# Performance work log

Measured on AMD Instinct MI355X. Metric: run time of the kernel, lower is better.

Reference implementation:

```python
import jax, jax.numpy as jnp
import numpy as np

EMBED_DIM = 1024
NUM_HEADS = 16
HEAD_DIM = EMBED_DIM // NUM_HEADS


def setup_inputs() -> dict:
    key = jax.random.key(0)
    ks = jax.random.split(key, 9)
    B, T, D = 2, 4096, EMBED_DIM
    scale = 1.0 / np.sqrt(D)
    x = jax.random.normal(ks[0], (B, T, D), dtype=jnp.float32)
    # nn.Linear weights stored as (out, in); we use (in, out) layout via transpose-free init
    Wq = jax.random.uniform(ks[1], (D, D), dtype=jnp.float32, minval=-scale, maxval=scale)
    Wk = jax.random.uniform(ks[2], (D, D), dtype=jnp.float32, minval=-scale, maxval=scale)
    Wv = jax.random.uniform(ks[3], (D, D), dtype=jnp.float32, minval=-scale, maxval=scale)
    Wo = jax.random.uniform(ks[4], (D, D), dtype=jnp.float32, minval=-scale, maxval=scale)
    bq = jax.random.uniform(ks[5], (D,), dtype=jnp.float32, minval=-scale, maxval=scale)
    bk = jax.random.uniform(ks[6], (D,), dtype=jnp.float32, minval=-scale, maxval=scale)
    bv = jax.random.uniform(ks[7], (D,), dtype=jnp.float32, minval=-scale, maxval=scale)
    bo = jax.random.uniform(ks[8], (D,), dtype=jnp.float32, minval=-scale, maxval=scale)
    return {"x": x, "Wq": Wq, "bq": bq, "Wk": Wk, "bk": bk,
            "Wv": Wv, "bv": bv, "Wo": Wo, "bo": bo}


def reference(x, Wq, bq, Wk, bk, Wv, bv, Wo, bo):
    B, T, D = x.shape
    H, Hd = NUM_HEADS, HEAD_DIM
    q = x @ Wq + bq  # [B,T,D]
    k = x @ Wk + bk
    v = x @ Wv + bv
    # [B,T,D] -> [B,H,T,Hd]
    q = q.reshape(B, T, H, Hd).transpose(0, 2, 1, 3)
    k = k.reshape(B, T, H, Hd).transpose(0, 2, 1, 3)
    v = v.reshape(B, T, H, Hd).transpose(0, 2, 1, 3)
    att = jnp.einsum('bhqd,bhkd->bhqk', q, k) / jnp.sqrt(jnp.float32(Hd))
    causal = jnp.tril(jnp.ones((T, T), dtype=bool))  # True = keep
    att = jnp.where(causal, att, -jnp.inf)
    att = jax.nn.softmax(att, axis=-1)
    out = jnp.einsum('bhqk,bhkd->bhqd', att, v)  # [B,H,T,Hd]
    out = out.transpose(0, 2, 1, 3).reshape(B, T, D)
    return out @ Wo + bo
```

## Files before the change

kernel.cpp:

```cpp
#include <hip/hip_runtime.h>
#include <hip/hip_bf16.h>
#include <math.h>

typedef __bf16 bf16;
typedef __attribute__((ext_vector_type(8))) __bf16 bf16x8;
typedef __attribute__((ext_vector_type(4))) __bf16 bf16x4;
typedef __attribute__((ext_vector_type(4))) short short4v;
typedef __attribute__((ext_vector_type(4))) float f32x4;

#define MFMA16(a,b,c)  __builtin_amdgcn_mfma_f32_16x16x32_bf16((a),(b),(c),0,0,0)
#define MFMAK16(a,b,c) __builtin_amdgcn_mfma_f32_16x16x16bf16_1k((a),(b),(c),0,0,0)

__device__ __forceinline__ void gload16(const void* gp, void* lp) {
  __builtin_amdgcn_global_load_lds(
      (const __attribute__((address_space(1))) void*)gp,
      (__attribute__((address_space(3))) void*)lp, 16, 0, 0);
}

__global__ __launch_bounds__(256) void cast_x(
    const float* __restrict__ x, bf16* __restrict__ xb)
{
  size_t i = ((size_t)blockIdx.x*256 + threadIdx.x) * 8;
  f32x4 a = *(const f32x4*)(x+i);
  f32x4 b = *(const f32x4*)(x+i+4);
  bf16x8 o;
  #pragma unroll
  for (int j=0;j<4;j++) { o[j] = (bf16)a[j]; o[4+j] = (bf16)b[j]; }
  *(bf16x8*)(xb+i) = o;
}

__global__ __launch_bounds__(1024) void tr_cast(
    const float* __restrict__ w0, const float* __restrict__ w1,
    const float* __restrict__ w2, bf16* __restrict__ dst)
{
  __shared__ bf16 tile[64][65];
  const float* src = (blockIdx.z==0)?w0:(blockIdx.z==1)?w1:w2;
  bf16* d = dst + (size_t)blockIdx.z * (1024*1024);
  int x = threadIdx.x, y = threadIdx.y;
  int tc = blockIdx.x, tr = blockIdx.y;
  #pragma unroll
  for (int i=0;i<4;i++) {
    int r = y + i*16;
    tile[r][x] = (bf16)src[(size_t)(tr*64+r)*1024 + tc*64 + x];
  }
  __syncthreads();
  #pragma unroll
  for (int i=0;i<4;i++) {
    int r = y + i*16;
    d[(size_t)(tc*64+r)*1024 + tr*64 + x] = tile[x][r];
  }
}

__global__ __launch_bounds__(1024) void v_tr(
    const bf16* __restrict__ v, bf16* __restrict__ vt)
{
  __shared__ bf16 tile[64][65];
  int x = threadIdx.x, y = threadIdx.y;
  int tt = blockIdx.x;
  int bh = blockIdx.y;
  int b = bh >> 4, h = bh & 15;
  const bf16* src = v + ((size_t)b*4096 + tt*64)*1024 + h*64;
  bf16* dst = vt + ((size_t)bh*64)*4096 + tt*64;
  #pragma unroll
  for (int i=0;i<4;i++) {
    int r = y + i*16;
    tile[r][x] = src[(size_t)r*1024 + x];
  }
  __syncthreads();
  #pragma unroll
  for (int i=0;i<4;i++) {
    int r = y + i*16;
    dst[(size_t)r*4096 + x] = tile[x][r];
  }
}

__global__ __launch_bounds__(256) void gemm_qkv(
    const bf16* __restrict__ A, const bf16* __restrict__ Bt,
    const float* __restrict__ bq, const float* __restrict__ bk, const float* __restrict__ bv,
    bf16* __restrict__ q, bf16* __restrict__ k, bf16* __restrict__ v,
    int M, int K)
{
  __shared__ __align__(16) bf16 As[128*64];
  __shared__ __align__(16) bf16 Bs[128*64];
  const int tid  = threadIdx.x;
  const int wave = tid >> 6;
  const int lane = tid & 63;
  const int l15  = lane & 15;
  const int quad = lane >> 4;
  const int m0 = blockIdx.y * 128;
  const int n0 = blockIdx.x * 128;
  const int wm = (wave >> 1) * 64;
  const int wn = (wave & 1) * 64;

  int srow[4], scol[4];
  #pragma unroll
  for (int p=0;p<4;p++) {
    int cid = p*256 + tid;
    srow[p] = cid >> 3;
    scol[p] = ((cid & 7) ^ (srow[p] & 7)) << 3;
  }
  const int swz8 = l15 & 7;
  int rdo[2];
  #pragma unroll
  for (int kk=0;kk<2;kk++) rdo[kk] = (((kk*4 + quad) ^ swz8) << 3);

  f32x4 acc[4][4];
  #pragma unroll
  for (int i=0;i<4;i++)
    #pragma unroll
    for (int j=0;j<4;j++)
      acc[i][j] = (f32x4){0.f,0.f,0.f,0.f};

  for (int k0 = 0; k0 < K; k0 += 64) {
    __syncthreads();
    #pragma unroll
    for (int p=0;p<4;p++) {
      int cid = p*256 + tid;
      gload16(A  + (size_t)(m0+srow[p])*K + k0 + scol[p], As + cid*8);
      gload16(Bt + (size_t)(n0+srow[p])*K + k0 + scol[p], Bs + cid*8);
    }
    __syncthreads();
    #pragma unroll
    for (int kk=0;kk<2;kk++) {
      bf16x8 af[4], bfr[4];
      #pragma unroll
      for (int t=0;t<4;t++) {
        af[t]  = *(const bf16x8*)(As + (wm + t*16 + l15)*64 + rdo[kk]);
        bfr[t] = *(const bf16x8*)(Bs + (wn + t*16 + l15)*64 + rdo[kk]);
      }
      #pragma unroll
      for (int mt=0;mt<4;mt++)
        #pragma unroll
        for (int nt=0;nt<4;nt++)
          acc[mt][nt] = MFMA16(af[mt], bfr[nt], acc[mt][nt]);
    }
  }

  const int mat = n0 >> 10;
  const float* bsel = (mat==0) ? bq : (mat==1) ? bk : bv;
  bf16*       osel  = (mat==0) ? q  : (mat==1) ? k  : v;
  const float qsc   = (mat==0) ? 0.1803368801f : 1.0f;
  #pragma unroll
  for (int nt=0;nt<4;nt++) {
    int col = n0 + wn + nt*16 + l15;
    int cw  = col & 1023;
    float bvv = bsel[cw];
    #pragma unroll
    for (int mt=0;mt<4;mt++) {
      int row = m0 + wm + mt*16 + quad*4;
      #pragma unroll
      for (int r=0;r<4;r++)
        osel[(size_t)(row + r)*1024 + cw] = (bf16)((acc[mt][nt][r] + bvv) * qsc);
    }
  }
}

__global__ __launch_bounds__(256, 4) void gemm_out(
    const bf16* __restrict__ A, const bf16* __restrict__ Bt,
    const float* __restrict__ bias, float* __restrict__ C,
    int M, int N, int K)
{
  __shared__ __align__(16) bf16 As[128*64];
  __shared__ __align__(16) bf16 Bs[64*64];
  const int tid  = threadIdx.x;
  const int wave = tid >> 6;
  const int lane = tid & 63;
  const int l15  = lane & 15;
  const int quad = lane >> 4;
  const int m0 = blockIdx.y * 128;
  const int n0 = blockIdx.x * 64;
  const int wm = (wave >> 1) * 64;
  const int wn = (wave & 1) * 32;

  int srow[4], scol[4];
  #pragma unroll
  for (int p=0;p<4;p++) {
    int cid = p*256 + tid;
    srow[p] = cid >> 3;
    scol[p] = ((cid & 7) ^ (srow[p] & 7)) << 3;
  }
  const int swz8 = l15 & 7;
  int rdo[2];
  #pragma unroll
  for (int kk=0;kk<2;kk++) rdo[kk] = (((kk*4 + quad) ^ swz8) << 3);

  f32x4 acc[4][2];
  #pragma unroll
  for (int i=0;i<4;i++)
    #pragma unroll
    for (int j=0;j<2;j++)
      acc[i][j] = (f32x4){0.f,0.f,0.f,0.f};

  for (int k0 = 0; k0 < K; k0 += 64) {
    __syncthreads();
    #pragma unroll
    for (int p=0;p<4;p++)
      gload16(A + (size_t)(m0+srow[p])*K + k0 + scol[p], As + (p*256+tid)*8);
    #pragma unroll
    for (int p=0;p<2;p++) {
      int cid = p*256 + tid;
      gload16(Bt + (size_t)(n0+srow[p])*K + k0 + scol[p], Bs + cid*8);
    }
    __syncthreads();
    #pragma unroll
    for (int kk=0;kk<2;kk++) {
      bf16x8 af[4], bfr[2];
      #pragma unroll
      for (int t=0;t<4;t++)
        af[t]  = *(const bf16x8*)(As + (wm + t*16 + l15)*64 + rdo[kk]);
      #pragma unroll
      for (int t=0;t<2;t++)
        bfr[t] = *(const bf16x8*)(Bs + (wn + t*16 + l15)*64 + rdo[kk]);
      #pragma unroll
      for (int mt=0;mt<4;mt++)
        #pragma unroll
        for (int nt=0;nt<2;nt++)
          acc[mt][nt] = MFMA16(af[mt], bfr[nt], acc[mt][nt]);
    }
  }

  #pragma unroll
  for (int nt=0;nt<2;nt++) {
    int col = n0 + wn + nt*16 + l15;
    float bvv = bias[col];
    #pragma unroll
    for (int mt=0;mt<4;mt++) {
      int row = m0 + wm + mt*16 + quad*4;
      #pragma unroll
      for (int r=0;r<4;r++)
        C[(size_t)(row + r)*N + col] = acc[mt][nt][r] + bvv;
    }
  }
}

__global__ __launch_bounds__(256, 2) void attn_fwd(
    const bf16* __restrict__ Q, const bf16* __restrict__ Kp,
    const bf16* __restrict__ Vtg, bf16* __restrict__ O)
{
  __shared__ __align__(16) char KsB[4*8192];
  __shared__ __align__(16) char VtB[4*8192];

  const int tid  = threadIdx.x;
  const int w    = tid >> 6;
  const int lane = tid & 63;
  const int l15  = lane & 15;
  const int quad = lane >> 4;

  const int bid = blockIdx.x;
  const int pp  = bid >> 5;
  const int bh  = bid & 31;
  const int h   = bh & 15;
  const int b   = bh >> 4;

  const size_t headoff = (size_t)h * 64;
  const size_t bbase   = (size_t)b * 4096;

  short4v ones_s;
  {
    bf16x4 o1;
    #pragma unroll
    for (int j=0;j<4;j++) o1[j] = (bf16)1.0f;
    ones_s = __builtin_bit_cast(short4v, o1);
  }

  const int kt_row = tid >> 2;
  const int kswz   = (kt_row & 7) << 4;
  const int ks_w0  = kt_row*128 + (((tid & 3)*32)      ^ kswz);
  const int ks_w1  = kt_row*128 + (((tid & 3)*32 + 16) ^ kswz);

  const int vd  = tid >> 2;
  const int vt0 = (tid & 3) * 16;
  int vw[4];
  #pragma unroll
  for (int u=0;u<4;u++)
    vw[u] = vd*128 + (((vt0 + u*4)*2) ^ ((vd & 15) << 3));

  const int s7    = l15 & 7;
  const int ks_r0 = l15*128 + ((quad ^ (s7 & 3)) << 4) + ((s7 >> 2) << 6);
  const int ks_r1 = ks_r0 ^ 64;
  const int vt_rbase = l15*128 + ((quad ^ (l15 & 3)) << 3) + ((l15 >> 2) << 5);
  int vt_r[4];
  #pragma unroll
  for (int tt=0;tt<4;tt++) vt_r[tt] = vt_rbase ^ (tt << 5);

  const bf16* kbase0 = Kp  + (bbase + kt_row)*1024 + headoff + (tid & 3)*16;
  const bf16* vbase0 = Vtg + ((size_t)(bh*64) + vd)*4096 + vt0;

  for (int ph = 0; ph < 2; ++ph) {
    const int qt = ph ? (31 - pp) : pp;
    const int q0 = qt * 128;
    const int ktmax = 2*qt + 1;

    bf16x8 aqA[2], aqB[2];
    {
      int rowA = q0 + w*16 + l15;
      const bf16* qp = Q + (bbase + rowA)*1024 + headoff + quad*8;
      aqA[0] = *(const bf16x8*)(qp);
      aqA[1] = *(const bf16x8*)(qp + 32);
      qp += 64*1024;
      aqB[0] = *(const bf16x8*)(qp);
      aqB[1] = *(const bf16x8*)(qp + 32);
    }

    f32x4 accoA[4], accoB[4], accliA, accliB;
    #pragma unroll
    for (int i=0;i<4;i++) { accoA[i] = (f32x4){0.f,0.f,0.f,0.f}; accoB[i] = (f32x4){0.f,0.f,0.f,0.f}; }
    accliA = (f32x4){0.f,0.f,0.f,0.f};
    accliB = (f32x4){0.f,0.f,0.f,0.f};

    __syncthreads();
    #pragma unroll
    for (int j=0;j<2;j++) {
      const bf16* kp = kbase0 + (size_t)j*64*1024;
      const bf16* vp = vbase0 + j*64;
      bf16x8 k0 = *(const bf16x8*)(kp);
      bf16x8 k1 = *(const bf16x8*)(kp + 8);
      bf16x8 v0 = *(const bf16x8*)(vp);
      bf16x8 v1 = *(const bf16x8*)(vp + 8);
      char* ksn = KsB + j*8192;
      char* vtn = VtB + j*8192;
      *(bf16x8*)(ksn + ks_w0) = k0;
      *(bf16x8*)(ksn + ks_w1) = k1;
      *(bf16x4*)(vtn + vw[0]) = __builtin_shufflevector(v0, v0, 0,1,2,3);
      *(bf16x4*)(vtn + vw[1]) = __builtin_shufflevector(v0, v0, 4,5,6,7);
      *(bf16x4*)(vtn + vw[2]) = __builtin_shufflevector(v1, v1, 0,1,2,3);
      *(bf16x4*)(vtn + vw[3]) = __builtin_shufflevector(v1, v1, 4,5,6,7);
    }
    __syncthreads();

    const bf16* kpref = kbase0 + (size_t)2*64*1024;
    const bf16* vpref = vbase0 + 128;

    for (int kt = 0; kt <= ktmax; ++kt) {
      const bool pre = (kt + 2 <= ktmax);

      bf16x8 kr0, kr1, vr0, vr1;
      if (pre) {
        kr0 = *(const bf16x8*)(kpref);
        kr1 = *(const bf16x8*)(kpref + 8);
        vr0 = *(const bf16x8*)(vpref);
        vr1 = *(const bf16x8*)(vpref + 8);
        kpref += 64*1024;
        vpref += 64;
      }

      const char* ksb = KsB + (kt & 3)*8192;
      const char* vtb = VtB + (kt & 3)*8192;

      f32x4 accsA[4], accsB[4];
      #pragma unroll
      for (int i=0;i<4;i++) { accsA[i] = (f32x4){0.f,0.f,0.f,0.f}; accsB[i] = (f32x4){0.f,0.f,0.f,0.f}; }

      __builtin_amdgcn_s_setprio(1);
      #pragma unroll
      for (int kk=0;kk<2;kk++) {
        #pragma unroll
        for (int tt=0;tt<4;tt++) {
          bf16x8 ka = *(const bf16x8*)(ksb + (kk ? ks_r1 : ks_r0) + tt*2048);
          accsA[tt] = MFMA16(ka, aqA[kk], accsA[tt]);
          accsB[tt] = MFMA16(ka, aqB[kk], accsB[tt]);
        }
      }
      __builtin_amdgcn_s_setprio(0);

      short4v ptsA[4], ptsB[4];
      if (kt < 2*qt) {
        #pragma unroll
        for (int tt=0;tt<4;tt++) {
          bf16x4 pa, pb;
          #pragma unroll
          for (int r=0;r<4;r++) {
            pa[r] = (bf16)__builtin_amdgcn_exp2f(accsA[tt][r]);
            pb[r] = (bf16)__builtin_amdgcn_exp2f(accsB[tt][r]);
          }
          ptsA[tt] = __builtin_bit_cast(short4v, pa);
          ptsB[tt] = __builtin_bit_cast(short4v, pb);
        }
      } else {
        const bool adead = (kt > 2*qt);
        #pragma unroll
        for (int tt=0;tt<4;tt++) {
          bf16x4 pa, pb;
          #pragma unroll
          for (int r=0;r<4;r++) {
            const bool tq = (tt*16 + quad*4 + r > w*16 + l15);
            float fa = __builtin_amdgcn_exp2f(accsA[tt][r]);
            if (adead || tq) fa = 0.0f;
            float fb = __builtin_amdgcn_exp2f(accsB[tt][r]);
            if (adead && tq) fb = 0.0f;
            pa[r] = (bf16)fa; pb[r] = (bf16)fb;
          }
          ptsA[tt] = __builtin_bit_cast(short4v, pa);
          ptsB[tt] = __builtin_bit_cast(short4v, pb);
        }
      }

      __builtin_amdgcn_s_setprio(1);
      #pragma unroll
      for (int nt=0;nt<4;nt++) {
        #pragma unroll
        for (int tt=0;tt<4;tt++) {
          bf16x4 va = *(const bf16x4*)(vtb + vt_r[tt] + nt*2048);
          short4v vas = __builtin_bit_cast(short4v, va);
          accoA[nt] = MFMAK16(vas, ptsA[tt], accoA[nt]);
          accoB[nt] = MFMAK16(vas, ptsB[tt], accoB[nt]);
        }
      }
      #pragma unroll
      for (int tt=0;tt<4;tt++) {
        accliA = MFMAK16(ones_s, ptsA[tt], accliA);
        accliB = MFMAK16(ones_s, ptsB[tt], accliB);
      }
      __builtin_amdgcn_s_setprio(0);

      if (pre) {
        char* ksn = KsB + ((kt + 2) & 3)*8192;
        char* vtn = VtB + ((kt + 2) & 3)*8192;
        *(bf16x8*)(ksn + ks_w0) = kr0;
        *(bf16x8*)(ksn + ks_w1) = kr1;
        *(bf16x4*)(vtn + vw[0]) = __builtin_shufflevector(vr0, vr0, 0,1,2,3);
        *(bf16x4*)(vtn + vw[1]) = __builtin_shufflevector(vr0, vr0, 4,5,6,7);
        *(bf16x4*)(vtn + vw[2]) = __builtin_shufflevector(vr1, vr1, 0,1,2,3);
        *(bf16x4*)(vtn + vw[3]) = __builtin_shufflevector(vr1, vr1, 4,5,6,7);
      }
      if (kt & 1) __syncthreads();
    }

    {
      float invA = 1.0f / accliA[0];
      float invB = 1.0f / accliB[0];
      int rowA = q0 + w*16 + l15;
      bf16* obA = O + (bbase + rowA)*1024 + headoff;
      bf16* obB = obA + 64*1024;
      #pragma unroll
      for (int nt=0;nt<4;nt++) {
        bf16x4 oA, oB;
        #pragma unroll
        for (int r=0;r<4;r++) {
          oA[r] = (bf16)(accoA[nt][r] * invA);
          oB[r] = (bf16)(accoB[nt][r] * invB);
        }
        *(bf16x4*)(obA + nt*16 + quad*4) = oA;
        *(bf16x4*)(obB + nt*16 + quad*4) = oB;
      }
    }
  }
}

extern "C" void kernel_launch(void* const* d_in, const int* in_sizes, int n_in,
                              void* d_out, int out_size, void* d_ws, size_t ws_size,
                              hipStream_t stream) {
  const float* x  = (const float*)d_in[0];
  const float* Wq = (const float*)d_in[1];
  const float* bq = (const float*)d_in[2];
  const float* Wk = (const float*)d_in[3];
  const float* bk = (const float*)d_in[4];
  const float* Wv = (const float*)d_in[5];
  const float* bv = (const float*)d_in[6];
  const float* Wo = (const float*)d_in[7];
  const float* bo = (const float*)d_in[8];
  float* out = (float*)d_out;

  bf16* ws = (bf16*)d_ws;
  bf16* q  = ws;
  bf16* k  = q + (size_t)8192*1024;
  bf16* v  = k + (size_t)8192*1024;
  bf16* xb = v + (size_t)8192*1024;
  bf16* ao = q;
  bf16* WtQKV = (bf16*)d_out;
  bf16* vT    = (bf16*)d_out;
  bf16* WtO   = xb;

  tr_cast<<<dim3(16,16,3), dim3(64,16), 0, stream>>>(Wq, Wk, Wv, WtQKV);
  cast_x<<<4096, 256, 0, stream>>>(x, xb);
  gemm_qkv<<<dim3(24,64), 256, 0, stream>>>(xb, WtQKV, bq, bk, bv, q, k, v, 8192, 1024);
  v_tr<<<dim3(64,32), dim3(64,16), 0, stream>>>(v, vT);
  tr_cast<<<dim3(16,16,1), dim3(64,16), 0, stream>>>(Wo, Wo, Wo, WtO);
  attn_fwd<<<512, 256, 0, stream>>>(q, k, vT, ao);
  gemm_out<<<dim3(16,64), 256, 0, stream>>>(ao, WtO, bo, out, 8192, 1024, 1024);
}
```

Measured before the change: 295.7 us.

## Permute V-transpose layout for wide LDS reads and replace ones-MFMA row sums

The V transpose kernel now writes each 64-token group in a permuted column order. This lets the attention kernel store V tiles to LDS with two 16-byte writes using the same swizzle as K, and read 8 bf16 per lane to feed two MFMAs, instead of four 8-byte writes and 4-element reads. The softmax row sum is no longer computed with extra MFMAs against a ones vector. It is accumulated in scalar registers during the exp step and reduced with cross-lane shuffles at the end. This removes eight MFMAs per tile and halves the V LDS traffic instructions, at the cost of extra VALU adds and bf16-to-float conversions in the exp loop.

```diff
diff --git a/kernel.cpp b/kernel.cpp
--- a/kernel.cpp
+++ b/kernel.cpp
@@ -67,10 +67,11 @@
     tile[r][x] = src[(size_t)r*1024 + x];
   }
   __syncthreads();
+  const int c = ((x>>2)&3)*16 + (x>>4)*4 + (x&3);
   #pragma unroll
   for (int i=0;i<4;i++) {
     int r = y + i*16;
-    dst[(size_t)r*4096 + x] = tile[x][r];
+    dst[(size_t)r*4096 + c] = tile[x][r];
   }
 }
 
@@ -255,36 +256,18 @@
   const size_t headoff = (size_t)h * 64;
   const size_t bbase   = (size_t)b * 4096;
 
-  short4v ones_s;
-  {
-    bf16x4 o1;
-    #pragma unroll
-    for (int j=0;j<4;j++) o1[j] = (bf16)1.0f;
-    ones_s = __builtin_bit_cast(short4v, o1);
-  }
-
-  const int kt_row = tid >> 2;
-  const int kswz   = (kt_row & 7) << 4;
-  const int ks_w0  = kt_row*128 + (((tid & 3)*32)      ^ kswz);
-  const int ks_w1  = kt_row*128 + (((tid & 3)*32 + 16) ^ kswz);
-
-  const int vd  = tid >> 2;
-  const int vt0 = (tid & 3) * 16;
-  int vw[4];
-  #pragma unroll
-  for (int u=0;u<4;u++)
-    vw[u] = vd*128 + (((vt0 + u*4)*2) ^ ((vd & 15) << 3));
+  const int strow = tid >> 2;
+  const int sswz  = (strow & 7) << 4;
+  const int sw0   = strow*128 + (((tid & 3)*32)      ^ sswz);
+  const int sw1   = strow*128 + (((tid & 3)*32 + 16) ^ sswz);
 
   const int s7    = l15 & 7;
   const int ks_r0 = l15*128 + ((quad ^ (s7 & 3)) << 4) + ((s7 >> 2) << 6);
   const int ks_r1 = ks_r0 ^ 64;
-  const int vt_rbase = l15*128 + ((quad ^ (l15 & 3)) << 3) + ((l15 >> 2) << 5);
-  int vt_r[4];
-  #pragma unroll
-  for (int tt=0;tt<4;tt++) vt_r[tt] = vt_rbase ^ (tt << 5);
-
-  const bf16* kbase0 = Kp  + (bbase + kt_row)*1024 + headoff + (tid & 3)*16;
-  const bf16* vbase0 = Vtg + ((size_t)(bh*64) + vd)*4096 + vt0;
+  const int vt_rb = l15*128 + ((quad*32) ^ (s7 << 4));
+
+  const bf16* kbase0 = Kp  + (bbase + strow)*1024 + headoff + (tid & 3)*16;
+  const bf16* vbase0 = Vtg + ((size_t)(bh*64) + strow)*4096 + (tid & 3)*16;
 
   for (int ph = 0; ph < 2; ++ph) {
     const int qt = ph ? (31 - pp) : pp;
@@ -302,11 +285,10 @@
       aqB[1] = *(const bf16x8*)(qp + 32);
     }
 
-    f32x4 accoA[4], accoB[4], accliA, accliB;
+    f32x4 accoA[4], accoB[4];
+    float accliAf = 0.f, accliBf = 0.f;
     #pragma unroll
     for (int i=0;i<4;i++) { accoA[i] = (f32x4){0.f,0.f,0.f,0.f}; accoB[i] = (f32x4){0.f,0.f,0.f,0.f}; }
-    accliA = (f32x4){0.f,0.f,0.f,0.f};
-    accliB = (f32x4){0.f,0.f,0.f,0.f};
 
     __syncthreads();
     #pragma unroll
@@ -319,12 +301,10 @@
       bf16x8 v1 = *(const bf16x8*)(vp + 8);
       char* ksn = KsB + j*8192;
       char* vtn = VtB + j*8192;
-      *(bf16x8*)(ksn + ks_w0) = k0;
-      *(bf16x8*)(ksn + ks_w1) = k1;
-      *(bf16x4*)(vtn + vw[0]) = __builtin_shufflevector(v0, v0, 0,1,2,3);
-      *(bf16x4*)(vtn + vw[1]) = __builtin_shufflevector(v0, v0, 4,5,6,7);
-      *(bf16x4*)(vtn + vw[2]) = __builtin_shufflevector(v1, v1, 0,1,2,3);
-      *(bf16x4*)(vtn + vw[3]) = __builtin_shufflevector(v1, v1, 4,5,6,7);
+      *(bf16x8*)(ksn + sw0) = k0;
+      *(bf16x8*)(ksn + sw1) = k1;
+      *(bf16x8*)(vtn + sw0) = v0;
+      *(bf16x8*)(vtn + sw1) = v1;
     }
     __syncthreads();
 
@@ -372,6 +352,8 @@
           for (int r=0;r<4;r++) {
             pa[r] = (bf16)__builtin_amdgcn_exp2f(accsA[tt][r]);
             pb[r] = (bf16)__builtin_amdgcn_exp2f(accsB[tt][r]);
+            accliAf += (float)pa[r];
+            accliBf += (float)pb[r];
           }
           ptsA[tt] = __builtin_bit_cast(short4v, pa);
           ptsB[tt] = __builtin_bit_cast(short4v, pb);
@@ -389,6 +371,8 @@
             float fb = __builtin_amdgcn_exp2f(accsB[tt][r]);
             if (adead && tq) fb = 0.0f;
             pa[r] = (bf16)fa; pb[r] = (bf16)fb;
+            accliAf += (float)pa[r];
+            accliBf += (float)pb[r];
           }
           ptsA[tt] = __builtin_bit_cast(short4v, pa);
           ptsB[tt] = __builtin_bit_cast(short4v, pb);
@@ -399,36 +383,38 @@
       #pragma unroll
       for (int nt=0;nt<4;nt++) {
         #pragma unroll
-        for (int tt=0;tt<4;tt++) {
-          bf16x4 va = *(const bf16x4*)(vtb + vt_r[tt] + nt*2048);
-          short4v vas = __builtin_bit_cast(short4v, va);
-          accoA[nt] = MFMAK16(vas, ptsA[tt], accoA[nt]);
-          accoB[nt] = MFMAK16(vas, ptsB[tt], accoB[nt]);
+        for (int Tp=0;Tp<2;Tp++) {
+          bf16x8 vv = *(const bf16x8*)(vtb + nt*2048 + (vt_rb ^ (Tp<<4)));
+          short4v v0 = __builtin_bit_cast(short4v,
+              (bf16x4)__builtin_shufflevector(vv, vv, 0,1,2,3));
+          short4v v1 = __builtin_bit_cast(short4v,
+              (bf16x4)__builtin_shufflevector(vv, vv, 4,5,6,7));
+          accoA[nt] = MFMAK16(v0, ptsA[2*Tp],   accoA[nt]);
+          accoA[nt] = MFMAK16(v1, ptsA[2*Tp+1], accoA[nt]);
+          accoB[nt] = MFMAK16(v0, ptsB[2*Tp],   accoB[nt]);
+          accoB[nt] = MFMAK16(v1, ptsB[2*Tp+1], accoB[nt]);
         }
-      }
-      #pragma unroll
-      for (int tt=0;tt<4;tt++) {
-        accliA = MFMAK16(ones_s, ptsA[tt], accliA);
-        accliB = MFMAK16(ones_s, ptsB[tt], accliB);
       }
       __builtin_amdgcn_s_setprio(0);
 
       if (pre) {
         char* ksn = KsB + ((kt + 2) & 3)*8192;
         char* vtn = VtB + ((kt + 2) & 3)*8192;
-        *(bf16x8*)(ksn + ks_w0) = kr0;
-        *(bf16x8*)(ksn + ks_w1) = kr1;
-        *(bf16x4*)(vtn + vw[0]) = __builtin_shufflevector(vr0, vr0, 0,1,2,3);
-        *(bf16x4*)(vtn + vw[1]) = __builtin_shufflevector(vr0, vr0, 4,5,6,7);
-        *(bf16x4*)(vtn + vw[2]) = __builtin_shufflevector(vr1, vr1, 0,1,2,3);
-        *(bf16x4*)(vtn + vw[3]) = __builtin_shufflevector(vr1, vr1, 4,5,6,7);
+        *(bf16x8*)(ksn + sw0) = kr0;
+        *(bf16x8*)(ksn + sw1) = kr1;
+        *(bf16x8*)(vtn + sw0) = vr0;
+        *(bf16x8*)(vtn + sw1) = vr1;
       }
       if (kt & 1) __syncthreads();
     }
 
     {
-      float invA = 1.0f / accliA[0];
-      float invB = 1.0f / accliB[0];
+      accliAf += __shfl_xor(accliAf, 16);
+      accliAf += __shfl_xor(accliAf, 32);
+      accliBf += __shfl_xor(accliBf, 16);
+      accliBf += __shfl_xor(accliBf, 32);
+      float invA = 1.0f / accliAf;
+      float invB = 1.0f / accliBf;
       int rowA = q0 + w*16 + l15;
       bf16* obA = O + (bbase + rowA)*1024 + headoff;
       bf16* obB = obA + 64*1024;
```

Result: slower. 303.1 us (+2.5%).
